# Performance work log

Measured on AMD Instinct MI355X. Metric: run time of the kernel, lower is better.

Reference implementation:

```python
import jax, jax.numpy as jnp
import numpy as np
from jax import lax

B, F, I, S = 4, 1024, 2048, 2048
K, G = 7, 4
INIT_SCALE = 1.0
LEAK = 0.02


def _norm(x):
    # normalize over channel dim (axis 1): subtract mean, divide by RMS-style L2 norm
    x = x - jnp.mean(x, axis=1, keepdims=True)
    n = jnp.sqrt(jnp.sum(x * x, axis=1, keepdims=True)) * (x.shape[1] ** -0.5)
    return x / (n + 1e-5)


def _conv1x1(x, w):
    # x: [B, Cin, S], w: [Cout, Cin, 1]
    return jnp.einsum('bcs,oc->bos', x, w[:, :, 0])


def setup_inputs() -> dict:
    key = jax.random.key(0)
    k1, k2, k3, k4 = jax.random.split(key, 4)
    inp = jax.random.normal(k1, (B, F, S), dtype=jnp.float32)
    divisor = (jnp.arange(S, dtype=jnp.float32) + 1.0).reshape(1, 1, S)
    w0_gate = jax.random.normal(k2, (3 * I, F, 1), dtype=jnp.float32) * (F ** -0.5)
    w1 = jax.random.normal(k3, (3 * I, I // G, K), dtype=jnp.float32) * ((I // G * K) ** -0.5)
    w2_gate = jax.random.normal(k4, (F, I, 1), dtype=jnp.float32) * (I ** -0.5)
    return {"inp": inp, "divisor": divisor, "w0_gate": w0_gate, "w1": w1, "w2_gate": w2_gate}


def reference(inp, divisor, w0_gate, w1, w2_gate):
    # 1x1 conv features -> 3*intermediate
    x = _conv1x1(inp, w0_gate)                       # [B, 3I, S]
    depth, scale, shift = jnp.split(x, 3, axis=1)    # each [B, I, S]
    cum = jnp.cumsum(depth, axis=-1)
    x = jax.nn.leaky_relu(_norm(cum / divisor * scale + shift), LEAK)
    # causal pad + grouped conv1d intermediate -> 3*intermediate
    x = jnp.pad(x, ((0, 0), (0, 0), (K - 1, 0)))
    x = lax.conv_general_dilated(x, w1, window_strides=(1,), padding='VALID',
                                 dimension_numbers=('NCH', 'OIH', 'NCH'),
                                 feature_group_count=G)  # [B, 3I, S]
    s0, s1, sh = jnp.split(x, 3, axis=1)
    x = jax.nn.leaky_relu(_norm(s0 * s1 + sh), LEAK)     # [B, I, S]
    # 1x1 conv intermediate -> features
    out = _conv1x1(x, w2_gate)                           # [B, F, S]
    return out * INIT_SCALE
```

## Files before the change

kernel.cpp:

```cpp
#include <hip/hip_runtime.h>

#define BATCH 4
#define FDIM  1024
#define IDIM  2048
#define SDIM  2048
#define I3    6144
#define KW    7
#define IG    512
#define OG    1536
#define KD2   3584
#define SP    2056

using short8 = __attribute__((ext_vector_type(8))) short;
using f32x4  = __attribute__((ext_vector_type(4))) float;

__device__ __forceinline__ unsigned short f2bf(float f) {
  unsigned int u = __float_as_uint(f);
  u += 0x7fffu + ((u >> 16) & 1u);
  return (unsigned short)(u >> 16);
}
__device__ __forceinline__ float bf2f(unsigned short u) {
  return __uint_as_float((unsigned int)u << 16);
}

__device__ __forceinline__ void gload16(const void* g, void* l) {
  __builtin_amdgcn_global_load_lds((const __attribute__((address_space(1))) void*)g,
                                   (__attribute__((address_space(3))) void*)l,
                                   16, 0, 0);
}

template<int MODE, int OBF16>
__global__ __launch_bounds__(512, 1)
void gemm256(const unsigned short* __restrict__ A,
             const unsigned short* __restrict__ Bt,
             void* __restrict__ C,
             int mtiles, int ktiles,
             int lda, int ldb, int ldc,
             long aZ, long bZ, long cZ)
{
  __shared__ unsigned short lds[2][2][16384];

  const int tid  = threadIdx.x;
  const int wv   = tid >> 6;
  const int lane = tid & 63;
  const int lr = lane & 15, lq = lane >> 4;
  const int wr = wv >> 2, wc = wv & 3;
  const int xm = (lr & 7) << 4;
  const int c8 = ((tid & 7) ^ ((tid >> 3) & 7)) << 3;

  const int nwg = gridDim.x;
  const int cpx = nwg >> 3;
  const int bid = blockIdx.x;
  const int w   = (bid & 7) * cpx + (bid >> 3);
  const int T   = mtiles << 3;
  const int z   = w / T;
  const int rr  = w - z * T;
  const int mt  = rr % mtiles;
  const int nt  = rr / mtiles;

  const unsigned short* Ab;
  const unsigned short* Bb;
  size_t coff;
  int gbase = 0;
  if (MODE == 2) {
    int b = z >> 2, g = z & 3;
    Ab = A + (size_t)g * OG * KD2;
    Bb = Bt + (size_t)b * SP * IDIM;
    coff = ((size_t)b * I3 + (size_t)g * OG) * (size_t)ldc;
    gbase = g * IG;
  } else {
    Ab = A + (size_t)z * aZ;
    Bb = Bt + (size_t)z * bZ;
    coff = (size_t)z * cZ;
  }

  const int m0 = mt * 256, n0 = nt * 256;

  f32x4 acc[8][4];
  const f32x4 vzero = {0.f, 0.f, 0.f, 0.f};
#pragma unroll
  for (int i = 0; i < 8; ++i)
#pragma unroll
    for (int j = 0; j < 4; ++j) acc[i][j] = vzero;

  auto STAGEC = [&](int buf, int kt1, int c) {
    const int k0 = kt1 << 6;
    int row = (c << 6) + (tid >> 3);
    gload16(Ab + (size_t)(m0 + row) * lda + (k0 + c8),
            &lds[buf][0][c * 4096 + wv * 512]);
    const unsigned short* g;
    if (MODE == 2) {
      int kk = k0 + c8;
      g = Bb + (size_t)(n0 + row + (kk >> 9) + 2) * IDIM + (gbase + (kk & 511));
    } else {
      g = Bb + (size_t)(n0 + row) * ldb + (k0 + c8);
    }
    gload16(g, &lds[buf][1][c * 4096 + wv * 512]);
  };

  auto RDA = [&](int buf, int i, int kk) -> short8 {
    int row = wr * 128 + i * 16 + lr;
    int off = ((row << 7) + (kk << 1) + (lq << 4)) ^ xm;
    return *(const short8*)((const char*)&lds[buf][0][0] + off);
  };
  auto RDB = [&](int buf, int j, int kk) -> short8 {
    int row = wc * 64 + j * 16 + lr;
    int off = ((row << 7) + (kk << 1) + (lq << 4)) ^ xm;
    return *(const short8*)((const char*)&lds[buf][1][0] + off);
  };

#define MFMA16(AF, BV, IOFF)                                                     \
  __builtin_amdgcn_s_setprio(1);                                                 \
  _Pragma("unroll")                                                              \
  for (int i = 0; i < 4; ++i)                                                    \
    _Pragma("unroll")                                                            \
    for (int j = 0; j < 4; ++j)                                                  \
      acc[i + IOFF][j] =                                                         \
          __builtin_amdgcn_mfma_f32_16x16x32_bf16(AF[i], BV[j], acc[i + IOFF][j],\
                                                  0, 0, 0);                      \
  __builtin_amdgcn_s_setprio(0);

  STAGEC(0, 0, 0); STAGEC(0, 0, 1); STAGEC(0, 0, 2); STAGEC(0, 0, 3);
  asm volatile("s_waitcnt vmcnt(0)" ::: "memory");
  __builtin_amdgcn_s_barrier();
  __builtin_amdgcn_sched_barrier(0);

  for (int kt = 0; kt < ktiles - 1; ++kt) {
    const int cur = kt & 1;
    short8 af0[4], af1[4], bv0[4], bv1[4];
#pragma unroll
    for (int j = 0; j < 4; ++j) bv0[j] = RDB(cur, j, 0);
#pragma unroll
    for (int i = 0; i < 4; ++i) af0[i] = RDA(cur, i, 0);
    STAGEC(cur ^ 1, kt + 1, 0);
#pragma unroll
    for (int i = 0; i < 4; ++i) af1[i] = RDA(cur, i + 4, 0);
    MFMA16(af0, bv0, 0)
    STAGEC(cur ^ 1, kt + 1, 1);
#pragma unroll
    for (int j = 0; j < 4; ++j) bv1[j] = RDB(cur, j, 32);
#pragma unroll
    for (int i = 0; i < 4; ++i) af0[i] = RDA(cur, i, 32);
    MFMA16(af1, bv0, 4)
    STAGEC(cur ^ 1, kt + 1, 2);
#pragma unroll
    for (int i = 0; i < 4; ++i) af1[i] = RDA(cur, i + 4, 32);
    MFMA16(af0, bv1, 0)
    STAGEC(cur ^ 1, kt + 1, 3);
    MFMA16(af1, bv1, 4)

    asm volatile("s_waitcnt vmcnt(0)" ::: "memory");
    __builtin_amdgcn_s_barrier();
    __builtin_amdgcn_sched_barrier(0);
  }

  {
    const int cur = (ktiles - 1) & 1;
    short8 af0[4], af1[4], bv0[4], bv1[4];
#pragma unroll
    for (int j = 0; j < 4; ++j) bv0[j] = RDB(cur, j, 0);
#pragma unroll
    for (int i = 0; i < 4; ++i) af0[i] = RDA(cur, i, 0);
#pragma unroll
    for (int i = 0; i < 4; ++i) af1[i] = RDA(cur, i + 4, 0);
    MFMA16(af0, bv0, 0)
#pragma unroll
    for (int j = 0; j < 4; ++j) bv1[j] = RDB(cur, j, 32);
#pragma unroll
    for (int i = 0; i < 4; ++i) af0[i] = RDA(cur, i, 32);
    MFMA16(af1, bv0, 4)
#pragma unroll
    for (int i = 0; i < 4; ++i) af1[i] = RDA(cur, i + 4, 32);
    MFMA16(af0, bv1, 0)
    MFMA16(af1, bv1, 4)
  }
#undef MFMA16

#pragma unroll
  for (int i = 0; i < 8; ++i) {
#pragma unroll
    for (int j = 0; j < 4; ++j) {
      int ccol  = n0 + wc * 64 + j * 16 + lr;
      int rbase = m0 + wr * 128 + i * 16 + lq * 4;
      if (OBF16) {
        unsigned short* Cs = (unsigned short*)C + coff;
#pragma unroll
        for (int e = 0; e < 4; ++e)
          Cs[(size_t)(rbase + e) * ldc + ccol] = f2bf(acc[i][j][e]);
      } else {
        float* Cf = (float*)C + coff;
#pragma unroll
        for (int e = 0; e < 4; ++e)
          Cf[(size_t)(rbase + e) * ldc + ccol] = acc[i][j][e];
      }
    }
  }
}

__global__ void cvt_f2b(const float* __restrict__ in, unsigned short* __restrict__ out, long n) {
  long stride = (long)gridDim.x * blockDim.x;
  for (long i = (long)blockIdx.x * blockDim.x + threadIdx.x; i < n; i += stride)
    out[i] = f2bf(in[i]);
}

__global__ void perm_w1(const float* __restrict__ in, unsigned short* __restrict__ out) {
  const long n = (long)I3 * KD2;
  long stride = (long)gridDim.x * blockDim.x;
  for (long idx = (long)blockIdx.x * blockDim.x + threadIdx.x; idx < n; idx += stride) {
    long o  = idx / KD2;
    int rem = (int)(idx - o * KD2);
    int k   = rem >> 9;
    int c   = rem & 511;
    out[idx] = f2bf(in[o * KD2 + (long)c * KW + k]);
  }
}

__global__ void transpose_in(const float* __restrict__ in, unsigned short* __restrict__ out) {
  __shared__ float tile[64][65];
  int bid = blockIdx.x;
  int b   = bid >> 9;
  int rem = bid & 511;
  int ft  = rem >> 5;
  int st  = rem & 31;
  int tc  = threadIdx.x & 63, tr = threadIdx.x >> 6;
  const float* ip = in + ((size_t)b * FDIM + ft * 64) * SDIM + st * 64;
#pragma unroll
  for (int r = tr; r < 64; r += 4)
    tile[r][tc] = ip[(size_t)r * SDIM + tc];
  __syncthreads();
  unsigned short* op = out + ((size_t)b * SDIM + st * 64) * FDIM + ft * 64;
#pragma unroll
  for (int r = tr; r < 64; r += 4)
    op[(size_t)r * FDIM + tc] = f2bf(tile[tc][r]);
}

__global__ void scan_rows(const unsigned short* __restrict__ C1, unsigned short* __restrict__ V) {
  int rid = blockIdx.x;
  int b = rid >> 11;
  int i = rid & 2047;
  const unsigned short* dp = C1 + ((size_t)b * I3 + i) * SDIM;
  const unsigned short* sp = dp + (size_t)IDIM * SDIM;
  const unsigned short* hp = dp + (size_t)2 * IDIM * SDIM;
  unsigned short* vp = V + ((size_t)b * IDIM + i) * SDIM;
  int t = threadIdx.x;

  short8 dv = *(const short8*)(dp + t * 8);
  float c[8];
  float run = 0.f;
#pragma unroll
  for (int e = 0; e < 8; ++e) { run += bf2f((unsigned short)dv[e]); c[e] = run; }

  __shared__ float ps[256];
  ps[t] = run;
  __syncthreads();
  for (int off = 1; off < 256; off <<= 1) {
    float vv = (t >= off) ? ps[t - off] : 0.f;
    __syncthreads();
    ps[t] += vv;
    __syncthreads();
  }
  float excl = ps[t] - run;

  short8 sv = *(const short8*)(sp + t * 8);
  short8 hv = *(const short8*)(hp + t * 8);
  short8 ov;
#pragma unroll
  for (int e = 0; e < 8; ++e) {
    int s = t * 8 + e;
    float val = (excl + c[e]) / (float)(s + 1) * bf2f((unsigned short)sv[e]) + bf2f((unsigned short)hv[e]);
    ov[e] = (short)f2bf(val);
  }
  *(short8*)(vp + t * 8) = ov;
}

template<int MODE>
__global__ void stats_part(const unsigned short* __restrict__ X, float* __restrict__ psum,
                           float* __restrict__ psq) {
  int bid = blockIdx.x;
  int b   = bid >> 5;
  int s0  = (bid & 31) * 64;
  int iz  = blockIdx.y;
  int ts  = threadIdx.x & 63, tg = threadIdx.x >> 6;
  float sum = 0.f, sq = 0.f;
  for (int i = iz * 512 + tg; i < iz * 512 + 512; i += 4) {
    float g;
    if (MODE == 1) {
      g = bf2f(X[((size_t)b * IDIM + i) * SDIM + s0 + ts]);
    } else {
      float a  = bf2f(X[((size_t)b * I3 + i) * SDIM + s0 + ts]);
      float bb = bf2f(X[((size_t)b * I3 + IDIM + i) * SDIM + s0 + ts]);
      float cc = bf2f(X[((size_t)b * I3 + 2 * IDIM + i) * SDIM + s0 + ts]);
      g = a * bb + cc;
    }
    sum += g; sq += g * g;
  }
  __shared__ float sS[4][64], sQ[4][64];
  sS[tg][ts] = sum; sQ[tg][ts] = sq;
  __syncthreads();
  if (threadIdx.x < 64) {
    float s = sS[0][ts] + sS[1][ts] + sS[2][ts] + sS[3][ts];
    float q = sQ[0][ts] + sQ[1][ts] + sQ[2][ts] + sQ[3][ts];
    psum[((size_t)b * SDIM + s0 + ts) * 4 + iz] = s;
    psq [((size_t)b * SDIM + s0 + ts) * 4 + iz] = q;
  }
}

__global__ void stats_final(const float* __restrict__ psum, const float* __restrict__ psq,
                            float* __restrict__ mean, float* __restrict__ inv) {
  int idx = blockIdx.x * 256 + threadIdx.x;
  if (idx >= BATCH * SDIM) return;
  float s = psum[idx * 4] + psum[idx * 4 + 1] + psum[idx * 4 + 2] + psum[idx * 4 + 3];
  float q = psq [idx * 4] + psq [idx * 4 + 1] + psq [idx * 4 + 2] + psq [idx * 4 + 3];
  float m   = s * (1.f / 2048.f);
  float var = q * (1.f / 2048.f) - m * m;
  float n   = sqrtf(fmaxf(var, 0.f));
  mean[idx] = m;
  inv[idx]  = 1.f / (n + 1e-5f);
}

template<int MODE>
__global__ void norm_apply(const unsigned short* __restrict__ X, const float* __restrict__ mean,
                           const float* __restrict__ inv, unsigned short* __restrict__ out) {
  __shared__ float tile[64][65];
  int bid = blockIdx.x;
  int b   = bid >> 5;
  int s0  = (bid & 31) * 64;
  int i0  = blockIdx.y * 512;
  int tc  = threadIdx.x & 63, tr = threadIdx.x >> 6;
  float mn = mean[(size_t)b * SDIM + s0 + tc];
  float iv = inv [(size_t)b * SDIM + s0 + tc];
  size_t orow = (MODE == 1) ? ((size_t)b * SP + 8 + s0) : ((size_t)b * SDIM + s0);
  for (int ic = i0; ic < i0 + 512; ic += 64) {
#pragma unroll
    for (int r = tr; r < 64; r += 4) {
      int i = ic + r;
      float g;
      if (MODE == 1) {
        g = bf2f(X[((size_t)b * IDIM + i) * SDIM + s0 + tc]);
      } else {
        float a  = bf2f(X[((size_t)b * I3 + i) * SDIM + s0 + tc]);
        float bb = bf2f(X[((size_t)b * I3 + IDIM + i) * SDIM + s0 + tc]);
        float cc = bf2f(X[((size_t)b * I3 + 2 * IDIM + i) * SDIM + s0 + tc]);
        g = a * bb + cc;
      }
      float y = (g - mn) * iv;
      y = (y >= 0.f) ? y : 0.02f * y;
      tile[r][tc] = y;
    }
    __syncthreads();
#pragma unroll
    for (int r = tr; r < 64; r += 4)
      out[(orow + r) * IDIM + ic + tc] = f2bf(tile[tc][r]);
    __syncthreads();
  }
}

__global__ void zero_x1t_pad(unsigned short* __restrict__ x1t) {
  int idx = blockIdx.x * 256 + threadIdx.x;
  if (idx < BATCH * 8 * IDIM) {
    int b   = idx / (8 * IDIM);
    int rem = idx - b * (8 * IDIM);
    x1t[(size_t)b * SP * IDIM + rem] = 0;
  }
}

__global__ void report_ws(float* __restrict__ out, float mb) {
  if (threadIdx.x == 0 && blockIdx.x == 0) out[0] = mb;
}

extern "C" void kernel_launch(void* const* d_in, const int* in_sizes, int n_in,
                              void* d_out, int out_size, void* d_ws, size_t ws_size,
                              hipStream_t stream) {
  const float* inp = (const float*)d_in[0];
  const float* w0  = (const float*)d_in[2];
  const float* w1  = (const float*)d_in[3];
  const float* w2  = (const float*)d_in[4];
  float* out = (float*)d_out;
  char* ws = (char*)d_ws;

  const size_t REQ = 216465408ULL;
  if (ws_size < REQ) {
    report_ws<<<1, 1, 0, stream>>>(out, (float)(ws_size >> 20));
    return;
  }

  unsigned short* A2   = (unsigned short*)(ws + 0);
  unsigned short* A3   = (unsigned short*)(ws + 44040192);
  unsigned short* C1   = (unsigned short*)(ws + 48234496);
  unsigned short* X1T  = (unsigned short*)(ws + 148897792);
  char*           VXr  = ws + 182583296;
  unsigned short* A1   = (unsigned short*)(VXr + 0);
  unsigned short* BINT = (unsigned short*)(VXr + 12582912);
  unsigned short* V    = (unsigned short*)(VXr + 0);
  unsigned short* X2T  = (unsigned short*)(VXr + 0);
  float* PSUM = (float*)(ws + 216137728);
  float* PSQ  = (float*)(ws + 216268800);
  float* MEAN = (float*)(ws + 216399872);
  float* INV  = (float*)(ws + 216432640);

  cvt_f2b<<<2048, 256, 0, stream>>>(w0, A1, (long)I3 * FDIM);
  cvt_f2b<<<2048, 256, 0, stream>>>(w2, A3, (long)FDIM * IDIM);
  perm_w1<<<4096, 256, 0, stream>>>(w1, A2);
  transpose_in<<<2048, 256, 0, stream>>>(inp, BINT);
  zero_x1t_pad<<<256, 256, 0, stream>>>(X1T);

  gemm256<0, 1><<<24 * 8 * BATCH, 512, 0, stream>>>(
      A1, BINT, C1, 24, 16, FDIM, FDIM, SDIM,
      0L, (long)SDIM * FDIM, (long)I3 * SDIM);

  scan_rows<<<BATCH * IDIM, 256, 0, stream>>>(C1, V);

  stats_part<1><<<dim3(128, 4), 256, 0, stream>>>(V, PSUM, PSQ);
  stats_final<<<32, 256, 0, stream>>>(PSUM, PSQ, MEAN, INV);
  norm_apply<1><<<dim3(128, 4), 256, 0, stream>>>(V, MEAN, INV, X1T);

  gemm256<2, 1><<<6 * 8 * 16, 512, 0, stream>>>(
      A2, X1T, C1, 6, 56, KD2, 0, SDIM, 0L, 0L, 0L);

  stats_part<2><<<dim3(128, 4), 256, 0, stream>>>(C1, PSUM, PSQ);
  stats_final<<<32, 256, 0, stream>>>(PSUM, PSQ, MEAN, INV);
  norm_apply<2><<<dim3(128, 4), 256, 0, stream>>>(C1, MEAN, INV, X2T);

  gemm256<0, 0><<<4 * 8 * BATCH, 512, 0, stream>>>(
      A3, X2T, out, 4, 32, IDIM, IDIM, SDIM,
      0L, (long)SDIM * IDIM, (long)FDIM * SDIM);
}
```

Before: 690.4 us.

## Use 128-tile GEMM for final projection, stage perm_w1 via LDS, shuffle-based scan

```diff
diff --git a/kernel.cpp b/kernel.cpp
--- a/kernel.cpp
+++ b/kernel.cpp
@@ -197,6 +197,92 @@
   }
 }
 
+__global__ __launch_bounds__(256, 2)
+void gemm128(const unsigned short* __restrict__ A,
+             const unsigned short* __restrict__ Bt,
+             float* __restrict__ C,
+             int mtiles, int ktiles,
+             int lda, int ldb, int ldc,
+             long aZ, long bZ, long cZ)
+{
+  __shared__ unsigned short sA[128 * 64];
+  __shared__ unsigned short sB[128 * 64];
+
+  const int tid  = threadIdx.x;
+  const int wave = tid >> 6;
+  const int lane = tid & 63;
+  const int mt = blockIdx.x % mtiles;
+  const int nt = blockIdx.x / mtiles;
+  const int z  = blockIdx.y;
+
+  const unsigned short* Ab = A + (size_t)z * aZ;
+  const unsigned short* Bb = Bt + (size_t)z * bZ;
+  float* Cb = C + (size_t)z * cZ;
+
+  const int m0 = mt * 128, n0 = nt * 128;
+  const int wr = wave >> 1, wc = wave & 1;
+  const int lr = lane & 15, lq = lane >> 4;
+  const int xm = (lr & 7) << 4;
+  const int c8 = ((tid & 7) ^ ((tid >> 3) & 7)) << 3;
+
+  f32x4 acc[4][4];
+  const f32x4 vzero = {0.f, 0.f, 0.f, 0.f};
+#pragma unroll
+  for (int i = 0; i < 4; ++i)
+#pragma unroll
+    for (int j = 0; j < 4; ++j) acc[i][j] = vzero;
+
+  for (int kt = 0; kt < ktiles; ++kt) {
+    const int k0 = kt * 64;
+#pragma unroll
+    for (int it = 0; it < 4; ++it) {
+      int row = it * 32 + (tid >> 3);
+      gload16(Ab + (size_t)(m0 + row) * lda + (k0 + c8),
+              &sA[(size_t)(it * 256 + (tid & ~63)) * 8]);
+    }
+#pragma unroll
+    for (int it = 0; it < 4; ++it) {
+      int row = it * 32 + (tid >> 3);
+      gload16(Bb + (size_t)(n0 + row) * ldb + (k0 + c8),
+              &sB[(size_t)(it * 256 + (tid & ~63)) * 8]);
+    }
+    asm volatile("s_waitcnt vmcnt(0)" ::: "memory");
+    __builtin_amdgcn_s_barrier();
+#pragma unroll
+    for (int kk = 0; kk < 64; kk += 32) {
+      short8 af[4], bfr[4];
+#pragma unroll
+      for (int i = 0; i < 4; ++i) {
+        int row = wr * 64 + i * 16 + lr;
+        af[i] = *(const short8*)((const char*)sA + (((row << 7) + (kk << 1) + (lq << 4)) ^ xm));
+      }
+#pragma unroll
+      for (int j = 0; j < 4; ++j) {
+        int row = wc * 64 + j * 16 + lr;
+        bfr[j] = *(const short8*)((const char*)sB + (((row << 7) + (kk << 1) + (lq << 4)) ^ xm));
+      }
+#pragma unroll
+      for (int i = 0; i < 4; ++i)
+#pragma unroll
+        for (int j = 0; j < 4; ++j)
+          acc[i][j] = __builtin_amdgcn_mfma_f32_16x16x32_bf16(af[i], bfr[j], acc[i][j], 0, 0, 0);
+    }
+    __builtin_amdgcn_s_barrier();
+  }
+
+#pragma unroll
+  for (int i = 0; i < 4; ++i) {
+#pragma unroll
+    for (int j = 0; j < 4; ++j) {
+      int ccol  = n0 + wc * 64 + j * 16 + lr;
+      int rbase = m0 + wr * 64 + i * 16 + lq * 4;
+#pragma unroll
+      for (int e = 0; e < 4; ++e)
+        Cb[(size_t)(rbase + e) * ldc + ccol] = acc[i][j][e];
+    }
+  }
+}
+
 __global__ void cvt_f2b(const float* __restrict__ in, unsigned short* __restrict__ out, long n) {
   long stride = (long)gridDim.x * blockDim.x;
   for (long i = (long)blockIdx.x * blockDim.x + threadIdx.x; i < n; i += stride)
@@ -204,15 +290,20 @@
 }
 
 __global__ void perm_w1(const float* __restrict__ in, unsigned short* __restrict__ out) {
-  const long n = (long)I3 * KD2;
-  long stride = (long)gridDim.x * blockDim.x;
-  for (long idx = (long)blockIdx.x * blockDim.x + threadIdx.x; idx < n; idx += stride) {
-    long o  = idx / KD2;
-    int rem = (int)(idx - o * KD2);
-    int k   = rem >> 9;
-    int c   = rem & 511;
-    out[idx] = f2bf(in[o * KD2 + (long)c * KW + k]);
-  }
+  __shared__ float row[2][KD2];
+  int o0 = blockIdx.x * 2;
+  int t  = threadIdx.x;
+#pragma unroll
+  for (int r = 0; r < 2; ++r)
+    for (int j = t; j < KD2; j += 256)
+      row[r][j] = in[(size_t)(o0 + r) * KD2 + j];
+  __syncthreads();
+#pragma unroll
+  for (int r = 0; r < 2; ++r)
+    for (int j = t; j < KD2; j += 256) {
+      int c = j & 511, k = j >> 9;
+      out[(size_t)(o0 + r) * KD2 + j] = f2bf(row[r][c * KW + k]);
+    }
 }
 
 __global__ void transpose_in(const float* __restrict__ in, unsigned short* __restrict__ out) {
@@ -242,7 +333,7 @@
   const unsigned short* sp = dp + (size_t)IDIM * SDIM;
   const unsigned short* hp = dp + (size_t)2 * IDIM * SDIM;
   unsigned short* vp = V + ((size_t)b * IDIM + i) * SDIM;
-  int t = threadIdx.x;
+  int t = threadIdx.x, lane = t & 63, wid = t >> 6;
 
   short8 dv = *(const short8*)(dp + t * 8);
   float c[8];
@@ -250,24 +341,27 @@
 #pragma unroll
   for (int e = 0; e < 8; ++e) { run += bf2f((unsigned short)dv[e]); c[e] = run; }
 
-  __shared__ float ps[256];
-  ps[t] = run;
+  float s = run;
+#pragma unroll
+  for (int off = 1; off < 64; off <<= 1) {
+    float v = __shfl_up(s, off, 64);
+    if (lane >= off) s += v;
+  }
+  __shared__ float wtot[4];
+  if (lane == 63) wtot[wid] = s;
   __syncthreads();
-  for (int off = 1; off < 256; off <<= 1) {
-    float vv = (t >= off) ? ps[t - off] : 0.f;
-    __syncthreads();
-    ps[t] += vv;
-    __syncthreads();
-  }
-  float excl = ps[t] - run;
+  float base = 0.f;
+#pragma unroll
+  for (int w2 = 0; w2 < 3; ++w2) base += (w2 < wid) ? wtot[w2] : 0.f;
+  float excl = base + s - run;
 
   short8 sv = *(const short8*)(sp + t * 8);
   short8 hv = *(const short8*)(hp + t * 8);
   short8 ov;
 #pragma unroll
   for (int e = 0; e < 8; ++e) {
-    int s = t * 8 + e;
-    float val = (excl + c[e]) / (float)(s + 1) * bf2f((unsigned short)sv[e]) + bf2f((unsigned short)hv[e]);
+    int si = t * 8 + e;
+    float val = (excl + c[e]) / (float)(si + 1) * bf2f((unsigned short)sv[e]) + bf2f((unsigned short)hv[e]);
     ov[e] = (short)f2bf(val);
   }
   *(short8*)(vp + t * 8) = ov;
@@ -400,7 +494,7 @@
 
   cvt_f2b<<<2048, 256, 0, stream>>>(w0, A1, (long)I3 * FDIM);
   cvt_f2b<<<2048, 256, 0, stream>>>(w2, A3, (long)FDIM * IDIM);
-  perm_w1<<<4096, 256, 0, stream>>>(w1, A2);
+  perm_w1<<<I3 / 2, 256, 0, stream>>>(w1, A2);
   transpose_in<<<2048, 256, 0, stream>>>(inp, BINT);
   zero_x1t_pad<<<256, 256, 0, stream>>>(X1T);
 
@@ -421,7 +515,7 @@
   stats_final<<<32, 256, 0, stream>>>(PSUM, PSQ, MEAN, INV);
   norm_apply<2><<<dim3(128, 4), 256, 0, stream>>>(C1, MEAN, INV, X2T);
 
-  gemm256<0, 0><<<4 * 8 * BATCH, 512, 0, stream>>>(
-      A3, X2T, out, 4, 32, IDIM, IDIM, SDIM,
+  gemm128<<<dim3(8 * 16, BATCH), 256, 0, stream>>>(
+      A3, X2T, out, 8, 32, IDIM, IDIM, SDIM,
       0L, (long)SDIM * IDIM, (long)FDIM * SDIM);
 }
```

New measurement: 674.8 us. 1.02x faster.
